# Kernel tuning notes

Measured on AMD Instinct MI355X. Metric: run time of the kernel, lower is better.

Reference implementation:

```python
import jax, jax.numpy as jnp
import numpy as np

N = 50000      # num nodes
E = 500000     # num edges
D = 128        # in_dim == out_dim
H = 8          # num heads
DPH = D // H   # 16, out_dim_per_head
DFF = 2 * D    # FFN hidden
EPS_BN = 1e-5


def setup_inputs() -> dict:
    key = jax.random.key(0)
    ks = jax.random.split(key, 16)
    s = 0.05
    inp = {
        "x": jax.random.normal(ks[0], (N, D), dtype=jnp.float32),
        "edge_index": jax.random.randint(ks[1], (2, E), 0, N, dtype=jnp.int64),
        # attention projections (no bias, use_bias=False); stored as [in, out]
        "WQ": jax.random.normal(ks[2], (D, D), dtype=jnp.float32) * s,
        "WK": jax.random.normal(ks[3], (D, D), dtype=jnp.float32) * s,
        "WV": jax.random.normal(ks[4], (D, D), dtype=jnp.float32) * s,
        # output projection O (has bias by default)
        "WO": jax.random.normal(ks[5], (D, D), dtype=jnp.float32) * s,
        "bO": jnp.zeros((D,), dtype=jnp.float32),
        # FFN
        "W1": jax.random.normal(ks[6], (D, DFF), dtype=jnp.float32) * s,
        "b1": jnp.zeros((DFF,), dtype=jnp.float32),
        "W2": jax.random.normal(ks[7], (DFF, D), dtype=jnp.float32) * s,
        "b2": jnp.zeros((D,), dtype=jnp.float32),
        # batch norms (affine)
        "g1": jnp.ones((D,), dtype=jnp.float32),
        "be1": jnp.zeros((D,), dtype=jnp.float32),
        "g2": jnp.ones((D,), dtype=jnp.float32),
        "be2": jnp.zeros((D,), dtype=jnp.float32),
    }
    return inp


def _batch_norm(h, g, b):
    # training-mode BatchNorm1d over node (batch) dim, biased variance
    mu = jnp.mean(h, axis=0)
    var = jnp.var(h, axis=0)
    return g * (h - mu) * jax.lax.rsqrt(var + EPS_BN) + b


def _forward(x, edge_index, WQ, WK, WV, WO, bO, W1, b1, W2, b2, g1, be1, g2, be2):
    src = edge_index[0]  # j (source / neighbor)
    dst = edge_index[1]  # i (target, softmax segment index)

    Q = (x @ WQ).reshape(N, H, DPH)
    K = (x @ WK).reshape(N, H, DPH)
    V = (x @ WV).reshape(N, H, DPH)

    # edge-wise scores: [E, H]
    score = jnp.sum(Q[dst] * K[src], axis=-1) / jnp.sqrt(jnp.float32(DPH))
    score = jnp.clip(score, -5.0, 5.0)

    # segment softmax over edges grouped by destination node (per head)
    seg_max = jax.ops.segment_max(score, dst, num_segments=N)      # [N, H]
    seg_max = jnp.where(jnp.isfinite(seg_max), seg_max, 0.0)       # empty segs
    ex = jnp.exp(score - seg_max[dst])                             # [E, H]
    seg_sum = jax.ops.segment_sum(ex, dst, num_segments=N)         # [N, H]
    alpha = ex / (seg_sum[dst] + 1e-16)                            # [E, H]

    # weighted message + scatter-add aggregation
    msg = V[src] * alpha[..., None]                                # [E, H, DPH]
    agg = jax.ops.segment_sum(msg, dst, num_segments=N)            # [N, H, DPH]
    h = agg.reshape(N, D)

    # output projection + residual (in_dim == out_dim, no proj) + BN
    h = h @ WO + bO
    h = x + h
    h = _batch_norm(h, g1, be1)

    # FFN + residual + BN
    h2 = h
    h = jax.nn.relu(h @ W1 + b1)
    h = h @ W2 + b2
    h = h2 + h
    h = _batch_norm(h, g2, be2)
    return h


def reference(x, edge_index, WQ, WK, WV, WO, bO, W1, b1, W2, b2, g1, be1, g2, be2):
    return _forward(x, edge_index, WQ, WK, WV, WO, bO, W1, b1, W2, b2, g1, be1, g2, be2)
```

## Files before the change

### kernel.cpp

```cpp
#include <hip/hip_runtime.h>

#define DEV __device__ __forceinline__

constexpr int N = 50000;
constexpr int E = 500000;
constexpr int D = 128;
constexpr int DFF = 256;
constexpr int NBANK = 64;

typedef __attribute__((ext_vector_type(8))) short bfrag8;
typedef __attribute__((ext_vector_type(4))) float f32x4;

DEV unsigned short f2b(float f) {
    unsigned u = __float_as_uint(f);
    unsigned r = (u + 0x7FFFu + ((u >> 16) & 1u)) >> 16;
    return (unsigned short)r;
}
DEV unsigned pack2(float a, float b) {
    return (unsigned)f2b(a) | ((unsigned)f2b(b) << 16);
}
DEV float b2f(unsigned short v) { return __uint_as_float(((unsigned)v) << 16); }
DEV float lo16(unsigned u) { return __uint_as_float(u << 16); }
DEV float hi16(unsigned u) { return __uint_as_float(u & 0xFFFF0000u); }

constexpr float QSCALE = 0.36067376022224085f;
constexpr float CLIP2 = 7.2134752044448170f;

constexpr size_t AL(size_t x) { return (x + 511) & ~(size_t)511; }
constexpr size_t OFF_COUNTS = 0;
constexpr size_t OFF_CURSORS = AL(OFF_COUNTS + (size_t)N * 4);
constexpr size_t OFF_BANK1 = AL(OFF_CURSORS + (size_t)N * 4);
constexpr size_t OFF_BANK2 = AL(OFF_BANK1 + NBANK * 256 * 4);
constexpr size_t OFF_DONE = OFF_BANK2 + NBANK * 256 * 4;
constexpr size_t ZERO_END = OFF_DONE + 512;
constexpr size_t ZW = ZERO_END / 4;
constexpr size_t OFF_OFFS = AL(ZERO_END);
constexpr size_t OFF_BSUM = AL(OFF_OFFS + (size_t)N * 4);
constexpr size_t OFF_BPREF = AL(OFF_BSUM + 1024);
constexpr size_t OFF_SS1 = AL(OFF_BPREF + 1024);
constexpr size_t OFF_SS2 = AL(OFF_SS1 + 1024);
constexpr size_t OFF_B1P = AL(OFF_SS2 + 1024);
constexpr size_t OFF_CSR = AL(OFF_B1P + 1024);
constexpr size_t OFF_WQKVP = AL(OFF_CSR + (size_t)E * 4);
constexpr size_t OFF_WOP = AL(OFF_WQKVP + 49152 * 2);
constexpr size_t OFF_W1PF = AL(OFF_WOP + 16384 * 2);
constexpr size_t OFF_W1P = AL(OFF_W1PF + 32768 * 4);
constexpr size_t OFF_W2P = AL(OFF_W1P + 32768 * 2);
constexpr size_t OFF_Q = AL(OFF_W2P + 32768 * 2);
constexpr size_t OFF_KV = AL(OFF_Q + (size_t)N * 128 * 2);
constexpr size_t OFF_AGG = AL(OFF_KV + (size_t)N * 256 * 2);
constexpr size_t OFF_Y = AL(OFF_AGG + (size_t)N * 128 * 2);
constexpr size_t OFF_T = AL(OFF_Y + (size_t)N * 128 * 2);
constexpr size_t OFF_XB = AL(OFF_T + (size_t)N * 128 * 2);

__global__ void prep_w(const float* __restrict__ WQ, const float* __restrict__ WK,
                       const float* __restrict__ WV, const float* __restrict__ WO,
                       const float* __restrict__ W1, const float* __restrict__ W2,
                       unsigned short* __restrict__ WQKVp, unsigned short* __restrict__ WOp,
                       float* __restrict__ W1pf, unsigned short* __restrict__ W2p,
                       unsigned* __restrict__ zbase) {
    if (blockIdx.x >= 512) {
        size_t i = (size_t)(blockIdx.x - 512) * 256 + threadIdx.x;
        if (i < ZW) zbase[i] = 0u;
        return;
    }
    int gid = blockIdx.x * 256 + threadIdx.x;
    if (gid < 49152) {
        int s = gid >> 14, r = gid & 16383;
        int nt = r >> 11, kb = (r >> 9) & 3, lane = (r >> 3) & 63, j = r & 7;
        int n = nt * 16 + (lane & 15);
        int k = kb * 32 + (lane >> 4) * 8 + j;
        const float* W = (s == 0) ? WQ : (s == 1) ? WK : WV;
        WQKVp[gid] = f2b(W[k * 128 + n]);
    } else if (gid < 65536) {
        int r = gid - 49152;
        int nt = r >> 11, kb = (r >> 9) & 3, lane = (r >> 3) & 63, j = r & 7;
        int n = nt * 16 + (lane & 15);
        int k = kb * 32 + (lane >> 4) * 8 + j;
        WOp[r] = f2b(WO[k * 128 + n]);
    } else if (gid < 98304) {
        int r = gid - 65536;
        int nt = r >> 11, kb = (r >> 9) & 3, lane = (r >> 3) & 63, j = r & 7;
        int n = nt * 16 + (lane & 15);
        int k = kb * 32 + (lane >> 4) * 8 + j;
        W1pf[r] = W1[k * 256 + n];
    } else {
        int r = gid - 98304;
        int nt = r >> 12, kb = (r >> 9) & 7, lane = (r >> 3) & 63, j = r & 7;
        int n = nt * 16 + (lane & 15);
        int k = kb * 32 + (lane >> 4) * 8 + j;
        W2p[r] = f2b(W2[k * 128 + n]);
    }
}

__global__ void scan_a(const int* __restrict__ counts, int* __restrict__ offs,
                       int* __restrict__ bsum, int* __restrict__ bpref,
                       int* __restrict__ done) {
    __shared__ int sm[256];
    __shared__ int ticket;
    int t = threadIdx.x;
    int gi = blockIdx.x * 256 + t;
    int v = (gi < N) ? counts[gi] : 0;
    sm[t] = v;
    __syncthreads();
    for (int o = 1; o < 256; o <<= 1) {
        int x = (t >= o) ? sm[t - o] : 0;
        __syncthreads();
        sm[t] += x;
        __syncthreads();
    }
    if (gi < N) offs[gi] = sm[t] - v;
    if (t == 255) bsum[blockIdx.x] = sm[255];
    __threadfence();
    if (t == 0) ticket = atomicAdd(done, 1);
    __syncthreads();
    if (ticket == (int)gridDim.x - 1) {
        int bv = (t < (int)gridDim.x) ? atomicAdd(&bsum[t], 0) : 0;
        sm[t] = bv;
        __syncthreads();
        for (int o = 1; o < 256; o <<= 1) {
            int x = (t >= o) ? sm[t - o] : 0;
            __syncthreads();
            sm[t] += x;
            __syncthreads();
        }
        bpref[t] = sm[t] - bv;
    }
}

__global__ void fill_k(const int* __restrict__ eidx, const int* __restrict__ offs,
                       const int* __restrict__ bpref,
                       int* __restrict__ cursors, int* __restrict__ csr) {
    int e = blockIdx.x * 256 + threadIdx.x;
    if (e < E) {
        int d = eidx[E + e];
        int p = atomicAdd(&cursors[d], 1);
        csr[offs[d] + bpref[d >> 8] + p] = eidx[e];
    }
}

__global__ __launch_bounds__(256) void qkv_k(const float* __restrict__ x,
                                             const unsigned short* __restrict__ WQKVp,
                                             unsigned short* __restrict__ q,
                                             unsigned short* __restrict__ kv,
                                             unsigned short* __restrict__ xb,
                                             const int* __restrict__ eidx,
                                             int* __restrict__ counts, int nqkv) {
    if ((int)blockIdx.x >= nqkv) {
        int e = ((int)blockIdx.x - nqkv) * 256 + threadIdx.x;
        if (e < E) atomicAdd(&counts[eidx[E + e]], 1);
        return;
    }
    __shared__ unsigned short As[64][136];
    __shared__ unsigned short Cs[64][136];
    const int tid = threadIdx.x;
    const int lane = tid & 63, wave = tid >> 6;
    const int quad = lane >> 4, l15 = lane & 15;
    const int wr = wave >> 1, wc = wave & 1;
    const int row0 = blockIdx.x * 64;

#pragma unroll
    for (int it = 0; it < 4; it++) {
        int c = tid + it * 256;
        int r = c >> 4, k8 = (c & 15) * 8;
        int grow = row0 + r;
        uint4 val = {0u, 0u, 0u, 0u};
        if (grow < N) {
            const float* ap = x + (size_t)grow * 128 + k8;
            float4 f0 = *(const float4*)ap;
            float4 f1 = *(const float4*)(ap + 4);
            val.x = pack2(f0.x, f0.y);
            val.y = pack2(f0.z, f0.w);
            val.z = pack2(f1.x, f1.y);
            val.w = pack2(f1.z, f1.w);
        }
        *(uint4*)&As[r][k8] = val;
    }
    __syncthreads();

#pragma unroll
    for (int j = 0; j < 4; j++) {
        int idx = tid + j * 256;
        int u = idx >> 4, col8 = (idx & 15) * 8;
        int grow = row0 + u;
        if (grow < N) *(uint4*)(xb + (size_t)grow * 128 + col8) = *(const uint4*)&As[u][col8];
    }

    for (int s = 0; s < 3; s++) {
        f32x4 acc[2][4];
#pragma unroll
        for (int i = 0; i < 2; i++)
#pragma unroll
            for (int j = 0; j < 4; j++) acc[i][j] = (f32x4){0.f, 0.f, 0.f, 0.f};
#pragma unroll
        for (int ks = 0; ks < 4; ks++) {
            int k0 = ks * 32 + quad * 8;
            bfrag8 a0 = *(const bfrag8*)&As[wr * 32 + l15][k0];
            bfrag8 a1 = *(const bfrag8*)&As[wr * 32 + 16 + l15][k0];
#pragma unroll
            for (int jn = 0; jn < 4; jn++) {
                int nt = wc * 4 + jn;
                bfrag8 b = *(const bfrag8*)(WQKVp + ((((size_t)s * 8 + nt) * 4 + ks) * 64 + lane) * 8);
                acc[0][jn] = __builtin_amdgcn_mfma_f32_16x16x32_bf16(a0, b, acc[0][jn], 0, 0, 0);
                acc[1][jn] = __builtin_amdgcn_mfma_f32_16x16x32_bf16(a1, b, acc[1][jn], 0, 0, 0);
            }
        }
        if (s) __syncthreads();
        float sc = (s == 0) ? QSCALE : 1.0f;
#pragma unroll
        for (int i = 0; i < 2; i++) {
            int rb = wr * 32 + i * 16 + quad * 4;
#pragma unroll
            for (int jn = 0; jn < 4; jn++) {
                int cl = wc * 64 + jn * 16 + l15;
#pragma unroll
                for (int r = 0; r < 4; r++) Cs[rb + r][cl] = f2b(acc[i][jn][r] * sc);
            }
        }
        __syncthreads();
#pragma unroll
        for (int j = 0; j < 4; j++) {
            int idx = tid + j * 256;
            int u = idx >> 4, col8 = (idx & 15) * 8;
            int grow = row0 + u;
            if (grow < N) {
                uint4 v = *(const uint4*)&Cs[u][col8];
                if (s == 0)
                    *(uint4*)(q + (size_t)grow * 128 + col8) = v;
                else
                    *(uint4*)(kv + (size_t)grow * 256 + (s == 2 ? 128 : 0) + col8) = v;
            }
        }
    }
}

__global__ __launch_bounds__(256) void attn_k(const unsigned short* __restrict__ qb,
                                              const unsigned short* __restrict__ kv,
                                              const int* __restrict__ csr,
                                              const int* __restrict__ offs,
                                              const int* __restrict__ bpref,
                                              const int* __restrict__ counts,
                                              unsigned short* __restrict__ agg) {
    const int wave = threadIdx.x >> 6;
    const int i = blockIdx.x * 4 + wave;
    if (i >= N) return;
    const int lane = threadIdx.x & 63;
    const int slot = lane >> 4;
    const int m = lane & 15;

    uint4 qv = *(const uint4*)(qb + (size_t)i * 128 + m * 8);
    const float q0 = lo16(qv.x), q1 = hi16(qv.x);
    const float q2 = lo16(qv.y), q3 = hi16(qv.y);
    const float q4 = lo16(qv.z), q5 = hi16(qv.z);
    const float q6 = lo16(qv.w), q7 = hi16(qv.w);

    int off = offs[i] + bpref[i >> 8];
    int deg = counts[i];
    const unsigned short* kvm = kv + m * 8;
    float s = 0.f;
    float a0 = 0.f, a1 = 0.f, a2 = 0.f, a3 = 0.f, a4 = 0.f, a5 = 0.f, a6 = 0.f, a7 = 0.f;

    for (int base = 0; base < deg; base += 64) {
        int rem = deg - base;
        if (rem > 64) rem = 64;
        int myj = (lane < rem) ? csr[off + base + lane] : 0;
        for (int e = 0; e < rem; e += 8) {
            int sA = e + slot;
            int jA = __shfl(myj, sA, 64);
            const unsigned short* pA = kvm + (size_t)jA * 256;
            uint4 kA = *(const uint4*)pA;
            uint4 vA = *(const uint4*)(pA + 128);
            bool two = (e + 4) < rem;
            float pdA = (q0 * lo16(kA.x) + q1 * hi16(kA.x)) + (q2 * lo16(kA.y) + q3 * hi16(kA.y)) +
                        (q4 * lo16(kA.z) + q5 * hi16(kA.z)) + (q6 * lo16(kA.w) + q7 * hi16(kA.w));
            pdA += __shfl_xor(pdA, 1, 64);
            float wA = exp2f(fminf(fmaxf(pdA, -CLIP2), CLIP2));
            wA = (sA < rem) ? wA : 0.f;
            if (two) {
                int sB = e + 4 + slot;
                int jB = __shfl(myj, sB, 64);
                const unsigned short* pB = kvm + (size_t)jB * 256;
                uint4 kB = *(const uint4*)pB;
                uint4 vB = *(const uint4*)(pB + 128);
                float pdB = (q0 * lo16(kB.x) + q1 * hi16(kB.x)) + (q2 * lo16(kB.y) + q3 * hi16(kB.y)) +
                            (q4 * lo16(kB.z) + q5 * hi16(kB.z)) + (q6 * lo16(kB.w) + q7 * hi16(kB.w));
                pdB += __shfl_xor(pdB, 1, 64);
                float wB = exp2f(fminf(fmaxf(pdB, -CLIP2), CLIP2));
                wB = (sB < rem) ? wB : 0.f;
                s += wA + wB;
                a0 += wA * lo16(vA.x) + wB * lo16(vB.x);
                a1 += wA * hi16(vA.x) + wB * hi16(vB.x);
                a2 += wA * lo16(vA.y) + wB * lo16(vB.y);
                a3 += wA * hi16(vA.y) + wB * hi16(vB.y);
                a4 += wA * lo16(vA.z) + wB * lo16(vB.z);
                a5 += wA * hi16(vA.z) + wB * hi16(vB.z);
                a6 += wA * lo16(vA.w) + wB * lo16(vB.w);
                a7 += wA * hi16(vA.w) + wB * hi16(vB.w);
            } else {
                s += wA;
                a0 += wA * lo16(vA.x);
                a1 += wA * hi16(vA.x);
                a2 += wA * lo16(vA.y);
                a3 += wA * hi16(vA.y);
                a4 += wA * lo16(vA.z);
                a5 += wA * hi16(vA.z);
                a6 += wA * lo16(vA.w);
                a7 += wA * hi16(vA.w);
            }
        }
    }
#define SLOTRED(v)                 \
    v += __shfl_xor(v, 16, 64);    \
    v += __shfl_xor(v, 32, 64);
    SLOTRED(s)
    SLOTRED(a0) SLOTRED(a1) SLOTRED(a2) SLOTRED(a3)
    SLOTRED(a4) SLOTRED(a5) SLOTRED(a6) SLOTRED(a7)
#undef SLOTRED
    float inv = 1.0f / (s + 1e-16f);
    if (slot == 0) {
        uint4 o;
        o.x = pack2(a0 * inv, a1 * inv);
        o.y = pack2(a2 * inv, a3 * inv);
        o.z = pack2(a4 * inv, a5 * inv);
        o.w = pack2(a6 * inv, a7 * inv);
        *(uint4*)(agg + (size_t)i * 128 + m * 8) = o;
    }
}

__global__ __launch_bounds__(256) void wo_k(const unsigned short* __restrict__ agg,
                                            const unsigned short* __restrict__ WOp,
                                            const unsigned short* __restrict__ xb,
                                            const float* __restrict__ bO,
                                            unsigned short* __restrict__ Yb,
                                            float* __restrict__ bank1) {
    __shared__ unsigned short As[64][136];
    __shared__ unsigned short Xb[64][136];
    __shared__ float Cf[256];
    const int tid = threadIdx.x;
    const int lane = tid & 63, wave = tid >> 6;
    const int quad = lane >> 4, l15 = lane & 15;
    const int wr = wave >> 1, wc = wave & 1;
    const int row0 = blockIdx.x * 64;

    Cf[tid] = 0.f;
#pragma unroll
    for (int it = 0; it < 4; it++) {
        int c = tid + it * 256;
        int r = c >> 4, k8 = (c & 15) * 8;
        int grow = row0 + r;
        uint4 val = {0u, 0u, 0u, 0u};
        uint4 xv = {0u, 0u, 0u, 0u};
        if (grow < N) {
            val = *(const uint4*)(agg + (size_t)grow * 128 + k8);
            xv = *(const uint4*)(xb + (size_t)grow * 128 + k8);
        }
        *(uint4*)&As[r][k8] = val;
        *(uint4*)&Xb[r][k8] = xv;
    }
    __syncthreads();

    f32x4 acc[2][4];
#pragma unroll
    for (int i = 0; i < 2; i++)
#pragma unroll
        for (int j = 0; j < 4; j++) acc[i][j] = (f32x4){0.f, 0.f, 0.f, 0.f};
#pragma unroll
    for (int ks = 0; ks < 4; ks++) {
        int k0 = ks * 32 + quad * 8;
        bfrag8 a0 = *(const bfrag8*)&As[wr * 32 + l15][k0];
        bfrag8 a1 = *(const bfrag8*)&As[wr * 32 + 16 + l15][k0];
#pragma unroll
        for (int jn = 0; jn < 4; jn++) {
            int nt = wc * 4 + jn;
            bfrag8 b = *(const bfrag8*)(WOp + (((size_t)nt * 4 + ks) * 64 + lane) * 8);
            acc[0][jn] = __builtin_amdgcn_mfma_f32_16x16x32_bf16(a0, b, acc[0][jn], 0, 0, 0);
            acc[1][jn] = __builtin_amdgcn_mfma_f32_16x16x32_bf16(a1, b, acc[1][jn], 0, 0, 0);
        }
    }
    __syncthreads();

    unsigned short(*Cs)[136] = As;
    float colS[4] = {0.f, 0.f, 0.f, 0.f}, colQ[4] = {0.f, 0.f, 0.f, 0.f};
#pragma unroll
    for (int i = 0; i < 2; i++) {
        int rb = wr * 32 + i * 16 + quad * 4;
#pragma unroll
        for (int jn = 0; jn < 4; jn++) {
            int cl = wc * 64 + jn * 16 + l15;
            float bv = bO[cl];
#pragma unroll
            for (int r = 0; r < 4; r++) {
                int rl = rb + r;
                float v = acc[i][jn][r] + bv + b2f(Xb[rl][cl]);
                Cs[rl][cl] = f2b(v);
                if (row0 + rl < N) {
                    colS[jn] += v;
                    colQ[jn] += v * v;
                }
            }
        }
    }
#pragma unroll
    for (int jn = 0; jn < 4; jn++) {
        float s = colS[jn], q = colQ[jn];
        s += __shfl_xor(s, 16, 64);
        q += __shfl_xor(q, 16, 64);
        s += __shfl_xor(s, 32, 64);
        q += __shfl_xor(q, 32, 64);
        if (quad == 0) {
            int cl = wc * 64 + jn * 16 + l15;
            atomicAdd(&Cf[cl], s);
            atomicAdd(&Cf[128 + cl], q);
        }
    }
    __syncthreads();
    atomicAdd(&bank1[(size_t)(blockIdx.x & (NBANK - 1)) * 256 + tid], Cf[tid]);
#pragma unroll
    for (int j = 0; j < 4; j++) {
        int idx = tid + j * 256;
        int u = idx >> 4, col8 = (idx & 15) * 8;
        int grow = row0 + u;
        if (grow < N) *(uint4*)(Yb + (size_t)grow * 128 + col8) = *(const uint4*)&Cs[u][col8];
    }
}

__global__ __launch_bounds__(256) void bnscale_k(const float* __restrict__ bank1,
                                                 const float* __restrict__ g, const float* __restrict__ be,
                                                 const float* __restrict__ W1, const float* __restrict__ b1,
                                                 const float* __restrict__ W1pf,
                                                 float* __restrict__ ss, float* __restrict__ b1p,
                                                 unsigned short* __restrict__ W1p) {
    __shared__ float sm[256];
    __shared__ float scl[128];
    __shared__ float shf[128];
    int t = threadIdx.x;
    float s = 0.f;
    for (int cp = 0; cp < NBANK; cp++) s += bank1[cp * 256 + t];
    sm[t] = s;
    __syncthreads();
    if (t < 128) {
        float mu = sm[t] * (1.f / N);
        float var = sm[128 + t] * (1.f / N) - mu * mu;
        float sc = g[t] * rsqrtf(var + 1e-5f);
        float sh = be[t] - mu * sc;
        scl[t] = sc;
        shf[t] = sh;
        if (blockIdx.x == 0) {
            ss[t] = sc;
            ss[128 + t] = sh;
        }
    }
    __syncthreads();
    int i = blockIdx.x * 256 + t;
    int k = ((i >> 9) & 3) * 32 + (((i >> 3) & 63) >> 4) * 8 + (i & 7);
    W1p[i] = f2b(W1pf[i] * scl[k]);
    if (blockIdx.x == 0) {
        float acc = b1[t];
#pragma unroll 4
        for (int kk = 0; kk < 128; kk++) acc += shf[kk] * W1[kk * 256 + t];
        b1p[t] = acc;
    }
}

__global__ __launch_bounds__(256) void ffn_k(const unsigned short* __restrict__ Yb,
                                             const unsigned short* __restrict__ W1p,
                                             const unsigned short* __restrict__ W2p,
                                             const float* __restrict__ ss1,
                                             const float* __restrict__ b1p,
                                             const float* __restrict__ b2,
                                             unsigned short* __restrict__ Tb,
                                             float* __restrict__ bank2) {
    __shared__ unsigned short As[64][136];
    __shared__ unsigned short Zs[64][264];
    __shared__ float Cf[640];
    const int tid = threadIdx.x;
    const int lane = tid & 63, wave = tid >> 6;
    const int quad = lane >> 4, l15 = lane & 15;
    const int wr = wave >> 1, wc = wave & 1;
    const int row0 = blockIdx.x * 64;

    Cf[tid] = ss1[tid];
    Cf[256 + tid] = b1p[tid];
    if (tid < 128) Cf[512 + tid] = b2[tid];
#pragma unroll
    for (int it = 0; it < 4; it++) {
        int c = tid + it * 256;
        int r = c >> 4, k8 = (c & 15) * 8;
        int grow = row0 + r;
        uint4 val = {0u, 0u, 0u, 0u};
        if (grow < N) val = *(const uint4*)(Yb + (size_t)grow * 128 + k8);
        *(uint4*)&As[r][k8] = val;
    }
    __syncthreads();

#pragma unroll
    for (int h = 0; h < 2; h++) {
        f32x4 acc[2][4];
#pragma unroll
        for (int i = 0; i < 2; i++)
#pragma unroll
            for (int j = 0; j < 4; j++) acc[i][j] = (f32x4){0.f, 0.f, 0.f, 0.f};
#pragma unroll
        for (int ks = 0; ks < 4; ks++) {
            int k0 = ks * 32 + quad * 8;
            bfrag8 a0 = *(const bfrag8*)&As[wr * 32 + l15][k0];
            bfrag8 a1 = *(const bfrag8*)&As[wr * 32 + 16 + l15][k0];
#pragma unroll
            for (int jn = 0; jn < 4; jn++) {
                int nt = h * 8 + wc * 4 + jn;
                bfrag8 b = *(const bfrag8*)(W1p + (((size_t)nt * 4 + ks) * 64 + lane) * 8);
                acc[0][jn] = __builtin_amdgcn_mfma_f32_16x16x32_bf16(a0, b, acc[0][jn], 0, 0, 0);
                acc[1][jn] = __builtin_amdgcn_mfma_f32_16x16x32_bf16(a1, b, acc[1][jn], 0, 0, 0);
            }
        }
#pragma unroll
        for (int i = 0; i < 2; i++) {
            int rb = wr * 32 + i * 16 + quad * 4;
#pragma unroll
            for (int jn = 0; jn < 4; jn++) {
                int gc = h * 128 + wc * 64 + jn * 16 + l15;
                float bv = Cf[256 + gc];
#pragma unroll
                for (int r = 0; r < 4; r++)
                    Zs[rb + r][gc] = f2b(fmaxf(acc[i][jn][r] + bv, 0.f));
            }
        }
    }
    __syncthreads();

    f32x4 acc2[2][4];
#pragma unroll
    for (int i = 0; i < 2; i++)
#pragma unroll
        for (int j = 0; j < 4; j++) acc2[i][j] = (f32x4){0.f, 0.f, 0.f, 0.f};
#pragma unroll
    for (int ks = 0; ks < 8; ks++) {
        int k0 = ks * 32 + quad * 8;
        bfrag8 a0 = *(const bfrag8*)&Zs[wr * 32 + l15][k0];
        bfrag8 a1 = *(const bfrag8*)&Zs[wr * 32 + 16 + l15][k0];
#pragma unroll
        for (int jn = 0; jn < 4; jn++) {
            int nt = wc * 4 + jn;
            bfrag8 b = *(const bfrag8*)(W2p + (((size_t)nt * 8 + ks) * 64 + lane) * 8);
            acc2[0][jn] = __builtin_amdgcn_mfma_f32_16x16x32_bf16(a0, b, acc2[0][jn], 0, 0, 0);
            acc2[1][jn] = __builtin_amdgcn_mfma_f32_16x16x32_bf16(a1, b, acc2[1][jn], 0, 0, 0);
        }
    }
    __syncthreads();

    unsigned short(*Ts)[136] = (unsigned short(*)[136]) & Zs[0][0];
    float colS[4] = {0.f, 0.f, 0.f, 0.f}, colQ[4] = {0.f, 0.f, 0.f, 0.f};
#pragma unroll
    for (int i = 0; i < 2; i++) {
        int rb = wr * 32 + i * 16 + quad * 4;
#pragma unroll
        for (int jn = 0; jn < 4; jn++) {
            int cl = wc * 64 + jn * 16 + l15;
            float s1v = Cf[cl], sh1v = Cf[128 + cl], b2v = Cf[512 + cl];
#pragma unroll
            for (int r = 0; r < 4; r++) {
                int rl = rb + r;
                float yv = b2f(As[rl][cl]);
                float v = acc2[i][jn][r] + b2v + yv * s1v + sh1v;
                Ts[rl][cl] = f2b(v);
                if (row0 + rl < N) {
                    colS[jn] += v;
                    colQ[jn] += v * v;
                }
            }
        }
    }
    __syncthreads();
    Cf[tid] = 0.f;
    __syncthreads();
#pragma unroll
    for (int jn = 0; jn < 4; jn++) {
        float s = colS[jn], q = colQ[jn];
        s += __shfl_xor(s, 16, 64);
        q += __shfl_xor(q, 16, 64);
        s += __shfl_xor(s, 32, 64);
        q += __shfl_xor(q, 32, 64);
        if (quad == 0) {
            int cl = wc * 64 + jn * 16 + l15;
            atomicAdd(&Cf[cl], s);
            atomicAdd(&Cf[128 + cl], q);
        }
    }
    __syncthreads();
    atomicAdd(&bank2[(size_t)(blockIdx.x & (NBANK - 1)) * 256 + tid], Cf[tid]);
#pragma unroll
    for (int j = 0; j < 4; j++) {
        int idx = tid + j * 256;
        int u = idx >> 4, col8 = (idx & 15) * 8;
        int grow = row0 + u;
        if (grow < N) *(uint4*)(Tb + (size_t)grow * 128 + col8) = *(const uint4*)&Ts[u][col8];
    }
}

__global__ void bnfin2_k(const float* __restrict__ bank2,
                         const float* __restrict__ g, const float* __restrict__ be,
                         float* __restrict__ ss) {
    __shared__ float sm[256];
    int t = threadIdx.x;
    float s = 0.f;
    for (int cp = 0; cp < NBANK; cp++) s += bank2[cp * 256 + t];
    sm[t] = s;
    __syncthreads();
    if (t < 128) {
        float mu = sm[t] * (1.f / N);
        float var = sm[128 + t] * (1.f / N) - mu * mu;
        float sc = g[t] * rsqrtf(var + 1e-5f);
        ss[t] = sc;
        ss[128 + t] = be[t] - mu * sc;
    }
}

__global__ void bnout_k(const unsigned short* __restrict__ T, const float* __restrict__ ss,
                        float* __restrict__ Out) {
    size_t idx = ((size_t)blockIdx.x * 256 + threadIdx.x) * 8;
    if (idx >= (size_t)N * 128) return;
    int c0 = (int)(idx & 127);
    uint4 tv = *(const uint4*)(T + idx);
    float f[8];
    f[0] = __uint_as_float(tv.x << 16);
    f[1] = __uint_as_float(tv.x & 0xFFFF0000u);
    f[2] = __uint_as_float(tv.y << 16);
    f[3] = __uint_as_float(tv.y & 0xFFFF0000u);
    f[4] = __uint_as_float(tv.z << 16);
    f[5] = __uint_as_float(tv.z & 0xFFFF0000u);
    f[6] = __uint_as_float(tv.w << 16);
    f[7] = __uint_as_float(tv.w & 0xFFFF0000u);
    float4 o0, o1;
    o0.x = f[0] * ss[c0 + 0] + ss[128 + c0 + 0];
    o0.y = f[1] * ss[c0 + 1] + ss[128 + c0 + 1];
    o0.z = f[2] * ss[c0 + 2] + ss[128 + c0 + 2];
    o0.w = f[3] * ss[c0 + 3] + ss[128 + c0 + 3];
    o1.x = f[4] * ss[c0 + 4] + ss[128 + c0 + 4];
    o1.y = f[5] * ss[c0 + 5] + ss[128 + c0 + 5];
    o1.z = f[6] * ss[c0 + 6] + ss[128 + c0 + 6];
    o1.w = f[7] * ss[c0 + 7] + ss[128 + c0 + 7];
    *(float4*)(Out + idx) = o0;
    *(float4*)(Out + idx + 4) = o1;
}

extern "C" void kernel_launch(void* const* d_in, const int* in_sizes, int n_in,
                              void* d_out, int out_size, void* d_ws, size_t ws_size,
                              hipStream_t stream) {
    const float* x = (const float*)d_in[0];
    const int* eidx = (const int*)d_in[1];
    const float* WQ = (const float*)d_in[2];
    const float* WK = (const float*)d_in[3];
    const float* WV = (const float*)d_in[4];
    const float* WO = (const float*)d_in[5];
    const float* bO = (const float*)d_in[6];
    const float* W1 = (const float*)d_in[7];
    const float* b1 = (const float*)d_in[8];
    const float* W2 = (const float*)d_in[9];
    const float* b2 = (const float*)d_in[10];
    const float* g1 = (const float*)d_in[11];
    const float* be1 = (const float*)d_in[12];
    const float* g2 = (const float*)d_in[13];
    const float* be2 = (const float*)d_in[14];
    float* out = (float*)d_out;

    char* ws = (char*)d_ws;
    int* counts = (int*)(ws + OFF_COUNTS);
    int* cursors = (int*)(ws + OFF_CURSORS);
    float* bank1 = (float*)(ws + OFF_BANK1);
    float* bank2 = (float*)(ws + OFF_BANK2);
    int* done = (int*)(ws + OFF_DONE);
    int* offs = (int*)(ws + OFF_OFFS);
    int* bsum = (int*)(ws + OFF_BSUM);
    int* bpref = (int*)(ws + OFF_BPREF);
    float* ss1 = (float*)(ws + OFF_SS1);
    float* ss2 = (float*)(ws + OFF_SS2);
    float* b1p = (float*)(ws + OFF_B1P);
    int* csr = (int*)(ws + OFF_CSR);
    unsigned short* WQKVp = (unsigned short*)(ws + OFF_WQKVP);
    unsigned short* WOp = (unsigned short*)(ws + OFF_WOP);
    float* W1pf = (float*)(ws + OFF_W1PF);
    unsigned short* W1p = (unsigned short*)(ws + OFF_W1P);
    unsigned short* W2p = (unsigned short*)(ws + OFF_W2P);
    unsigned short* qb = (unsigned short*)(ws + OFF_Q);
    unsigned short* kv = (unsigned short*)(ws + OFF_KV);
    unsigned short* agg = (unsigned short*)(ws + OFF_AGG);
    unsigned short* Yb = (unsigned short*)(ws + OFF_Y);
    unsigned short* Tb = (unsigned short*)(ws + OFF_T);
    unsigned short* xb = (unsigned short*)(ws + OFF_XB);

    const int ZB = (int)((ZW + 255) / 256);
    prep_w<<<512 + ZB, 256, 0, stream>>>(WQ, WK, WV, WO, W1, W2, WQKVp, WOp, W1pf, W2p,
                                         (unsigned*)ws);

    const int EB = (E + 255) / 256;
    const int MB64 = (N + 63) / 64;
    qkv_k<<<MB64 + EB, 256, 0, stream>>>(x, WQKVp, qb, kv, xb, eidx, counts, MB64);
    scan_a<<<196, 256, 0, stream>>>(counts, offs, bsum, bpref, done);
    fill_k<<<EB, 256, 0, stream>>>(eidx, offs, bpref, cursors, csr);
    attn_k<<<(N + 3) / 4, 256, 0, stream>>>(qb, kv, csr, offs, bpref, counts, agg);
    wo_k<<<MB64, 256, 0, stream>>>(agg, WOp, xb, bO, Yb, bank1);
    bnscale_k<<<128, 256, 0, stream>>>(bank1, g1, be1, W1, b1, W1pf, ss1, b1p, W1p);
    ffn_k<<<MB64, 256, 0, stream>>>(Yb, W1p, W2p, ss1, b1p, b2, Tb, bank2);
    bnfin2_k<<<1, 256, 0, stream>>>(bank2, g2, be2, ss2);
    bnout_k<<<(int)(((size_t)N * 128 / 8 + 255) / 256), 256, 0, stream>>>(Tb, ss2, out);
}
```

Before: 266.1 us.

## Fold BN finalize into last-block tails, apply BN1 on FFN input load

```diff
diff --git a/kernel.cpp b/kernel.cpp
--- a/kernel.cpp
+++ b/kernel.cpp
@@ -6,7 +6,7 @@
 constexpr int E = 500000;
 constexpr int D = 128;
 constexpr int DFF = 256;
-constexpr int NBANK = 64;
+constexpr int NBANK = 16;
 
 typedef __attribute__((ext_vector_type(8))) short bfrag8;
 typedef __attribute__((ext_vector_type(4))) float f32x4;
@@ -31,7 +31,7 @@
 constexpr size_t OFF_CURSORS = AL(OFF_COUNTS + (size_t)N * 4);
 constexpr size_t OFF_BANK1 = AL(OFF_CURSORS + (size_t)N * 4);
 constexpr size_t OFF_BANK2 = AL(OFF_BANK1 + NBANK * 256 * 4);
-constexpr size_t OFF_DONE = OFF_BANK2 + NBANK * 256 * 4;
+constexpr size_t OFF_DONE = AL(OFF_BANK2 + NBANK * 256 * 4);
 constexpr size_t ZERO_END = OFF_DONE + 512;
 constexpr size_t ZW = ZERO_END / 4;
 constexpr size_t OFF_OFFS = AL(ZERO_END);
@@ -39,12 +39,10 @@
 constexpr size_t OFF_BPREF = AL(OFF_BSUM + 1024);
 constexpr size_t OFF_SS1 = AL(OFF_BPREF + 1024);
 constexpr size_t OFF_SS2 = AL(OFF_SS1 + 1024);
-constexpr size_t OFF_B1P = AL(OFF_SS2 + 1024);
-constexpr size_t OFF_CSR = AL(OFF_B1P + 1024);
+constexpr size_t OFF_CSR = AL(OFF_SS2 + 1024);
 constexpr size_t OFF_WQKVP = AL(OFF_CSR + (size_t)E * 4);
 constexpr size_t OFF_WOP = AL(OFF_WQKVP + 49152 * 2);
-constexpr size_t OFF_W1PF = AL(OFF_WOP + 16384 * 2);
-constexpr size_t OFF_W1P = AL(OFF_W1PF + 32768 * 4);
+constexpr size_t OFF_W1P = AL(OFF_WOP + 16384 * 2);
 constexpr size_t OFF_W2P = AL(OFF_W1P + 32768 * 2);
 constexpr size_t OFF_Q = AL(OFF_W2P + 32768 * 2);
 constexpr size_t OFF_KV = AL(OFF_Q + (size_t)N * 128 * 2);
@@ -57,7 +55,7 @@
                        const float* __restrict__ WV, const float* __restrict__ WO,
                        const float* __restrict__ W1, const float* __restrict__ W2,
                        unsigned short* __restrict__ WQKVp, unsigned short* __restrict__ WOp,
-                       float* __restrict__ W1pf, unsigned short* __restrict__ W2p,
+                       unsigned short* __restrict__ W1p, unsigned short* __restrict__ W2p,
                        unsigned* __restrict__ zbase) {
     if (blockIdx.x >= 512) {
         size_t i = (size_t)(blockIdx.x - 512) * 256 + threadIdx.x;
@@ -83,7 +81,7 @@
         int nt = r >> 11, kb = (r >> 9) & 3, lane = (r >> 3) & 63, j = r & 7;
         int n = nt * 16 + (lane & 15);
         int k = kb * 32 + (lane >> 4) * 8 + j;
-        W1pf[r] = W1[k * 256 + n];
+        W1p[r] = f2b(W1[k * 256 + n]);
     } else {
         int r = gid - 98304;
         int nt = r >> 12, kb = (r >> 9) & 7, lane = (r >> 3) & 63, j = r & 7;
@@ -331,11 +329,16 @@
                                             const unsigned short* __restrict__ WOp,
                                             const unsigned short* __restrict__ xb,
                                             const float* __restrict__ bO,
+                                            const float* __restrict__ g1,
+                                            const float* __restrict__ be1,
                                             unsigned short* __restrict__ Yb,
-                                            float* __restrict__ bank1) {
+                                            float* __restrict__ bank1,
+                                            int* __restrict__ done2,
+                                            float* __restrict__ ss1) {
     __shared__ unsigned short As[64][136];
     __shared__ unsigned short Xb[64][136];
     __shared__ float Cf[256];
+    __shared__ int tkt;
     const int tid = threadIdx.x;
     const int lane = tid & 63, wave = tid >> 6;
     const int quad = lane >> 4, l15 = lane & 15;
@@ -422,43 +425,21 @@
         int grow = row0 + u;
         if (grow < N) *(uint4*)(Yb + (size_t)grow * 128 + col8) = *(const uint4*)&Cs[u][col8];
     }
-}
-
-__global__ __launch_bounds__(256) void bnscale_k(const float* __restrict__ bank1,
-                                                 const float* __restrict__ g, const float* __restrict__ be,
-                                                 const float* __restrict__ W1, const float* __restrict__ b1,
-                                                 const float* __restrict__ W1pf,
-                                                 float* __restrict__ ss, float* __restrict__ b1p,
-                                                 unsigned short* __restrict__ W1p) {
-    __shared__ float sm[256];
-    __shared__ float scl[128];
-    __shared__ float shf[128];
-    int t = threadIdx.x;
-    float s = 0.f;
-    for (int cp = 0; cp < NBANK; cp++) s += bank1[cp * 256 + t];
-    sm[t] = s;
-    __syncthreads();
-    if (t < 128) {
-        float mu = sm[t] * (1.f / N);
-        float var = sm[128 + t] * (1.f / N) - mu * mu;
-        float sc = g[t] * rsqrtf(var + 1e-5f);
-        float sh = be[t] - mu * sc;
-        scl[t] = sc;
-        shf[t] = sh;
-        if (blockIdx.x == 0) {
-            ss[t] = sc;
-            ss[128 + t] = sh;
-        }
-    }
-    __syncthreads();
-    int i = blockIdx.x * 256 + t;
-    int k = ((i >> 9) & 3) * 32 + (((i >> 3) & 63) >> 4) * 8 + (i & 7);
-    W1p[i] = f2b(W1pf[i] * scl[k]);
-    if (blockIdx.x == 0) {
-        float acc = b1[t];
-#pragma unroll 4
-        for (int kk = 0; kk < 128; kk++) acc += shf[kk] * W1[kk * 256 + t];
-        b1p[t] = acc;
+    __threadfence();
+    if (tid == 0) tkt = atomicAdd(done2, 1);
+    __syncthreads();
+    if (tkt == (int)gridDim.x - 1) {
+        float s = 0.f;
+        for (int cp = 0; cp < NBANK; cp++) s += atomicAdd(&bank1[cp * 256 + tid], 0.0f);
+        Cf[tid] = s;
+        __syncthreads();
+        if (tid < 128) {
+            float mu = Cf[tid] * (1.f / N);
+            float var = Cf[128 + tid] * (1.f / N) - mu * mu;
+            float sc = g1[tid] * rsqrtf(var + 1e-5f);
+            ss1[tid] = sc;
+            ss1[128 + tid] = be1[tid] - mu * sc;
+        }
     }
 }
 
@@ -466,13 +447,18 @@
                                              const unsigned short* __restrict__ W1p,
                                              const unsigned short* __restrict__ W2p,
                                              const float* __restrict__ ss1,
-                                             const float* __restrict__ b1p,
+                                             const float* __restrict__ b1,
                                              const float* __restrict__ b2,
+                                             const float* __restrict__ g2,
+                                             const float* __restrict__ be2,
                                              unsigned short* __restrict__ Tb,
-                                             float* __restrict__ bank2) {
+                                             float* __restrict__ bank2,
+                                             int* __restrict__ done3,
+                                             float* __restrict__ ss2) {
     __shared__ unsigned short As[64][136];
     __shared__ unsigned short Zs[64][264];
     __shared__ float Cf[640];
+    __shared__ int tkt;
     const int tid = threadIdx.x;
     const int lane = tid & 63, wave = tid >> 6;
     const int quad = lane >> 4, l15 = lane & 15;
@@ -480,15 +466,26 @@
     const int row0 = blockIdx.x * 64;
 
     Cf[tid] = ss1[tid];
-    Cf[256 + tid] = b1p[tid];
+    Cf[256 + tid] = b1[tid];
     if (tid < 128) Cf[512 + tid] = b2[tid];
+    __syncthreads();
 #pragma unroll
     for (int it = 0; it < 4; it++) {
         int c = tid + it * 256;
         int r = c >> 4, k8 = (c & 15) * 8;
         int grow = row0 + r;
         uint4 val = {0u, 0u, 0u, 0u};
-        if (grow < N) val = *(const uint4*)(Yb + (size_t)grow * 128 + k8);
+        if (grow < N) {
+            uint4 y = *(const uint4*)(Yb + (size_t)grow * 128 + k8);
+            val.x = pack2(lo16(y.x) * Cf[k8 + 0] + Cf[128 + k8 + 0],
+                          hi16(y.x) * Cf[k8 + 1] + Cf[128 + k8 + 1]);
+            val.y = pack2(lo16(y.y) * Cf[k8 + 2] + Cf[128 + k8 + 2],
+                          hi16(y.y) * Cf[k8 + 3] + Cf[128 + k8 + 3]);
+            val.z = pack2(lo16(y.z) * Cf[k8 + 4] + Cf[128 + k8 + 4],
+                          hi16(y.z) * Cf[k8 + 5] + Cf[128 + k8 + 5]);
+            val.w = pack2(lo16(y.w) * Cf[k8 + 6] + Cf[128 + k8 + 6],
+                          hi16(y.w) * Cf[k8 + 7] + Cf[128 + k8 + 7]);
+        }
         *(uint4*)&As[r][k8] = val;
     }
     __syncthreads();
@@ -556,12 +553,12 @@
 #pragma unroll
         for (int jn = 0; jn < 4; jn++) {
             int cl = wc * 64 + jn * 16 + l15;
-            float s1v = Cf[cl], sh1v = Cf[128 + cl], b2v = Cf[512 + cl];
+            float b2v = Cf[512 + cl];
 #pragma unroll
             for (int r = 0; r < 4; r++) {
                 int rl = rb + r;
                 float yv = b2f(As[rl][cl]);
-                float v = acc2[i][jn][r] + b2v + yv * s1v + sh1v;
+                float v = acc2[i][jn][r] + b2v + yv;
                 Ts[rl][cl] = f2b(v);
                 if (row0 + rl < N) {
                     colS[jn] += v;
@@ -595,23 +592,21 @@
         int grow = row0 + u;
         if (grow < N) *(uint4*)(Tb + (size_t)grow * 128 + col8) = *(const uint4*)&Ts[u][col8];
     }
-}
-
-__global__ void bnfin2_k(const float* __restrict__ bank2,
-                         const float* __restrict__ g, const float* __restrict__ be,
-                         float* __restrict__ ss) {
-    __shared__ float sm[256];
-    int t = threadIdx.x;
-    float s = 0.f;
-    for (int cp = 0; cp < NBANK; cp++) s += bank2[cp * 256 + t];
-    sm[t] = s;
-    __syncthreads();
-    if (t < 128) {
-        float mu = sm[t] * (1.f / N);
-        float var = sm[128 + t] * (1.f / N) - mu * mu;
-        float sc = g[t] * rsqrtf(var + 1e-5f);
-        ss[t] = sc;
-        ss[128 + t] = be[t] - mu * sc;
+    __threadfence();
+    if (tid == 0) tkt = atomicAdd(done3, 1);
+    __syncthreads();
+    if (tkt == (int)gridDim.x - 1) {
+        float s = 0.f;
+        for (int cp = 0; cp < NBANK; cp++) s += atomicAdd(&bank2[cp * 256 + tid], 0.0f);
+        Cf[tid] = s;
+        __syncthreads();
+        if (tid < 128) {
+            float mu = Cf[tid] * (1.f / N);
+            float var = Cf[128 + tid] * (1.f / N) - mu * mu;
+            float sc = g2[tid] * rsqrtf(var + 1e-5f);
+            ss2[tid] = sc;
+            ss2[128 + tid] = be2[tid] - mu * sc;
+        }
     }
 }
 
@@ -669,16 +664,16 @@
     float* bank1 = (float*)(ws + OFF_BANK1);
     float* bank2 = (float*)(ws + OFF_BANK2);
     int* done = (int*)(ws + OFF_DONE);
+    int* done2 = (int*)(ws + OFF_DONE + 64);
+    int* done3 = (int*)(ws + OFF_DONE + 128);
     int* offs = (int*)(ws + OFF_OFFS);
     int* bsum = (int*)(ws + OFF_BSUM);
     int* bpref = (int*)(ws + OFF_BPREF);
     float* ss1 = (float*)(ws + OFF_SS1);
     float* ss2 = (float*)(ws + OFF_SS2);
-    float* b1p = (float*)(ws + OFF_B1P);
     int* csr = (int*)(ws + OFF_CSR);
     unsigned short* WQKVp = (unsigned short*)(ws + OFF_WQKVP);
     unsigned short* WOp = (unsigned short*)(ws + OFF_WOP);
-    float* W1pf = (float*)(ws + OFF_W1PF);
     unsigned short* W1p = (unsigned short*)(ws + OFF_W1P);
     unsigned short* W2p = (unsigned short*)(ws + OFF_W2P);
     unsigned short* qb = (unsigned short*)(ws + OFF_Q);
@@ -689,7 +684,7 @@
     unsigned short* xb = (unsigned short*)(ws + OFF_XB);
 
     const int ZB = (int)((ZW + 255) / 256);
-    prep_w<<<512 + ZB, 256, 0, stream>>>(WQ, WK, WV, WO, W1, W2, WQKVp, WOp, W1pf, W2p,
+    prep_w<<<512 + ZB, 256, 0, stream>>>(WQ, WK, WV, WO, W1, W2, WQKVp, WOp, W1p, W2p,
                                          (unsigned*)ws);
 
     const int EB = (E + 255) / 256;
@@ -698,9 +693,7 @@
     scan_a<<<196, 256, 0, stream>>>(counts, offs, bsum, bpref, done);
     fill_k<<<EB, 256, 0, stream>>>(eidx, offs, bpref, cursors, csr);
     attn_k<<<(N + 3) / 4, 256, 0, stream>>>(qb, kv, csr, offs, bpref, counts, agg);
-    wo_k<<<MB64, 256, 0, stream>>>(agg, WOp, xb, bO, Yb, bank1);
-    bnscale_k<<<128, 256, 0, stream>>>(bank1, g1, be1, W1, b1, W1pf, ss1, b1p, W1p);
-    ffn_k<<<MB64, 256, 0, stream>>>(Yb, W1p, W2p, ss1, b1p, b2, Tb, bank2);
-    bnfin2_k<<<1, 256, 0, stream>>>(bank2, g2, be2, ss2);
+    wo_k<<<MB64, 256, 0, stream>>>(agg, WOp, xb, bO, g1, be1, Yb, bank1, done2, ss1);
+    ffn_k<<<MB64, 256, 0, stream>>>(Yb, W1p, W2p, ss1, b1, b2, g2, be2, Tb, bank2, done3, ss2);
     bnout_k<<<(int)(((size_t)N * 128 / 8 + 255) / 256), 256, 0, stream>>>(Tb, ss2, out);
 }
```

Result: slower. 397.2 us (+49.3%).
